# Performance work log

Measured on AMD Instinct MI355X. Metric: run time of the kernel, lower is better.

## Reference

```python
import jax, jax.numpy as jnp
import numpy as np


def _agcn(x, node_embeddings, weights_pool, bias_pool, supports):
    # per-node weights: [N, dim_in, dim_out]
    weights = jnp.einsum('nd,dio->nio', node_embeddings, weights_pool)
    bias = node_embeddings @ bias_pool  # [N, dim_out]
    x_g = jnp.einsum('nm,bmc->bnc', supports, x)  # adaptive-adjacency aggregation
    return jnp.einsum('bni,nio->bno', x_g, weights) + bias


def setup_inputs() -> dict:
    key = jax.random.key(0)
    ks = jax.random.split(key, 7)
    B, N, D_IN, D_OUT, E = 64, 4096, 64, 64, 16
    return {
        'x': jax.random.normal(ks[0], (B, N, D_IN), dtype=jnp.float32),
        'state': jax.random.normal(ks[1], (B, N, D_OUT), dtype=jnp.float32),
        'node_embeddings': jax.random.normal(ks[2], (N, E), dtype=jnp.float32),
        'gate_weights_pool': jax.random.normal(ks[3], (E, D_IN + D_OUT, 2 * D_OUT), dtype=jnp.float32) * 0.1,
        'gate_bias_pool': jax.random.normal(ks[4], (E, 2 * D_OUT), dtype=jnp.float32) * 0.1,
        'update_weights_pool': jax.random.normal(ks[5], (E, D_IN + D_OUT, D_OUT), dtype=jnp.float32) * 0.1,
        'update_bias_pool': jax.random.normal(ks[6], (E, D_OUT), dtype=jnp.float32) * 0.1,
    }


def reference(x, state, node_embeddings, gate_weights_pool, gate_bias_pool,
              update_weights_pool, update_bias_pool) -> jnp.ndarray:
    hidden_dim = state.shape[-1]
    # learned adjacency shared by both GCNs: softmax(relu(E E^T), axis=1)
    supports = jax.nn.softmax(jax.nn.relu(node_embeddings @ node_embeddings.T), axis=1)
    input_and_state = jnp.concatenate([x, state], axis=-1)  # [B,N,dim_in+hidden]
    z_r = jax.nn.sigmoid(_agcn(input_and_state, node_embeddings,
                               gate_weights_pool, gate_bias_pool, supports))
    z, r = z_r[..., :hidden_dim], z_r[..., hidden_dim:]
    candidate = jnp.concatenate([x, z * state], axis=-1)
    hc = jnp.tanh(_agcn(candidate, node_embeddings,
                        update_weights_pool, update_bias_pool, supports))
    h = r * state + (1.0 - r) * hc
    return h
```

## Files before the change

kernel.cpp:

```cpp
#include <hip/hip_runtime.h>

typedef float f32x4 __attribute__((ext_vector_type(4)));
typedef float f32x16 __attribute__((ext_vector_type(16)));
typedef _Float16 f16x8 __attribute__((ext_vector_type(8)));
typedef _Float16 f16x4 __attribute__((ext_vector_type(4)));
typedef _Float16 f16x2 __attribute__((ext_vector_type(2)));

typedef __attribute__((address_space(1))) const unsigned char gbyte;
typedef __attribute__((address_space(3))) unsigned char sbyte;
__device__ __forceinline__ void gload_lds16(const void* gp, void* lp) {
  __builtin_amdgcn_global_load_lds((gbyte*)gp, (sbyte*)lp, 16, 0, 0);
}

__global__ __launch_bounds__(256) void k_wpoolT(const float* __restrict__ gwp,
                                                const float* __restrict__ uwp,
                                                float* __restrict__ wtg,
                                                float* __restrict__ wtu) {
  int idx = blockIdx.x * 256 + threadIdx.x;
  if (idx < 16 * 128 * 128) {
    int d = idx >> 14, rem = idx & 16383, o = rem >> 7, i = rem & 127;
    wtg[idx] = gwp[(d << 14) + (i << 7) + o];
  } else {
    int j = idx - 16 * 128 * 128;
    if (j < 16 * 64 * 128) {
      int d = j >> 13, rem = j & 8191, o = rem >> 7, i = rem & 127;
      wtu[j] = uwp[(d << 13) + (i << 6) + o];
    }
  }
}

__global__ __launch_bounds__(256) void k_supports(const float* __restrict__ emb,
                                                  _Float16* __restrict__ S) {
  int n0 = blockIdx.x * 4, tid = threadIdx.x;
  __shared__ float e_sh[4][16];
  __shared__ float red[4][4];
  if (tid < 16) {
    int r = tid >> 2, part = tid & 3;
    f32x4 v = *reinterpret_cast<const f32x4*>(emb + (n0 + r) * 16 + part * 4);
    *reinterpret_cast<f32x4*>(&e_sh[r][part * 4]) = v;
  }
  __syncthreads();
  float v[4][16];
  float sum[4] = {0.f, 0.f, 0.f, 0.f};
#pragma unroll
  for (int i = 0; i < 16; i++) {
    int m = i * 256 + tid;
    const f32x4* em = reinterpret_cast<const f32x4*>(emb + m * 16);
    f32x4 e0 = em[0], e1 = em[1], e2 = em[2], e3 = em[3];
#pragma unroll
    for (int r = 0; r < 4; r++) {
      float acc = 0.f;
#pragma unroll
      for (int q = 0; q < 4; q++) acc += e_sh[r][q] * e0[q];
#pragma unroll
      for (int q = 0; q < 4; q++) acc += e_sh[r][4 + q] * e1[q];
#pragma unroll
      for (int q = 0; q < 4; q++) acc += e_sh[r][8 + q] * e2[q];
#pragma unroll
      for (int q = 0; q < 4; q++) acc += e_sh[r][12 + q] * e3[q];
      acc = fmaxf(acc, 0.f);
      float e = __expf(acc);
      v[r][i] = e;
      sum[r] += e;
    }
  }
#pragma unroll
  for (int r = 0; r < 4; r++)
#pragma unroll
    for (int off = 32; off > 0; off >>= 1) sum[r] += __shfl_down(sum[r], off);
  if ((tid & 63) == 0) {
#pragma unroll
    for (int r = 0; r < 4; r++) red[tid >> 6][r] = sum[r];
  }
  __syncthreads();
  float inv[4];
#pragma unroll
  for (int r = 0; r < 4; r++)
    inv[r] = 1.f / (red[0][r] + red[1][r] + red[2][r] + red[3][r]);
#pragma unroll
  for (int i = 0; i < 16; i++)
#pragma unroll
    for (int r = 0; r < 4; r++)
      S[(size_t)(n0 + r) * 4096 + i * 256 + tid] = (_Float16)(v[r][i] * inv[r]);
}

__global__ __launch_bounds__(256) void k_concat(const float* __restrict__ x,
                                                const float* __restrict__ st,
                                                _Float16* __restrict__ xs_t) {
  int m0 = blockIdx.x * 64, b = blockIdx.y, tid = threadIdx.x;
  __shared__ __attribute__((aligned(16))) _Float16 T[64][130];
#pragma unroll
  for (int i = 0; i < 16; i++) {
    int li = i * 256 + tid;
    int ml = li >> 6, c = li & 63;
    int base = (b * 4096 + m0 + ml) * 64 + c;
    T[ml][c] = (_Float16)x[base];
    T[ml][64 + c] = (_Float16)st[base];
  }
  __syncthreads();
  int cg = tid >> 3, mch = tid & 7;
#pragma unroll
  for (int cb = 0; cb < 4; cb++) {
    int c = cb * 32 + cg;
    f16x8 tmp;
#pragma unroll
    for (int j = 0; j < 8; j++) tmp[j] = T[mch * 8 + j][c];
    *reinterpret_cast<f16x8*>(&xs_t[(b * 128 + c) * 4096 + m0 + mch * 8]) = tmp;
  }
}

__global__ __launch_bounds__(512) void k_gemm(const _Float16* __restrict__ S,
                                              const _Float16* __restrict__ Xt,
                                              _Float16* __restrict__ Y) {
  int nt = blockIdx.x, b = blockIdx.y;
  int tid = threadIdx.x, lane = tid & 63, w = tid >> 6;
  int wr = w >> 1, wc = w & 1;
  __shared__ __attribute__((aligned(16))) _Float16 As[256 * 64];
  __shared__ __attribute__((aligned(16))) _Float16 Bs[128 * 64];
  const _Float16* Sb = S + (size_t)nt * 256 * 4096;
  const _Float16* Xb = Xt + (size_t)b * 128 * 4096;
  f32x16 acc[2][2];
#pragma unroll
  for (int fm = 0; fm < 2; fm++)
#pragma unroll
    for (int fn = 0; fn < 2; fn++)
#pragma unroll
      for (int q = 0; q < 16; q++) acc[fm][fn][q] = 0.f;

  int lrow = lane >> 3;
  int lcolsw = (((lane & 7) ^ lrow) * 8);
  int r32 = lane & 31, hi32 = lane >> 5;
  int swz = (r32 & 7) * 8;
  for (int k0 = 0; k0 < 4096; k0 += 64) {
    __syncthreads();
#pragma unroll
    for (int i = 0; i < 4; i++) {
      int j = w * 4 + i;
      int row = j * 8 + lrow;
      gload_lds16(Sb + (size_t)row * 4096 + k0 + lcolsw, &As[j * 512]);
    }
#pragma unroll
    for (int i = 0; i < 2; i++) {
      int j = w * 2 + i;
      int row = j * 8 + lrow;
      gload_lds16(Xb + (size_t)row * 4096 + k0 + lcolsw, &Bs[j * 512]);
    }
    __syncthreads();
#pragma unroll
    for (int kk = 0; kk < 4; kk++) {
      int col = (kk * 16 + hi32 * 8) ^ swz;
      f16x8 af[2], bf[2];
#pragma unroll
      for (int fm = 0; fm < 2; fm++)
        af[fm] = *reinterpret_cast<const f16x8*>(&As[(wr * 64 + fm * 32 + r32) * 64 + col]);
#pragma unroll
      for (int fn = 0; fn < 2; fn++)
        bf[fn] = *reinterpret_cast<const f16x8*>(&Bs[(wc * 64 + fn * 32 + r32) * 64 + col]);
#pragma unroll
      for (int fm = 0; fm < 2; fm++)
#pragma unroll
        for (int fn = 0; fn < 2; fn++)
          acc[fm][fn] = __builtin_amdgcn_mfma_f32_32x32x16_f16(af[fm], bf[fn], acc[fm][fn], 0, 0, 0);
    }
  }
#pragma unroll
  for (int fm = 0; fm < 2; fm++)
#pragma unroll
    for (int fn = 0; fn < 2; fn++)
#pragma unroll
      for (int reg = 0; reg < 16; reg++) {
        int row = nt * 256 + wr * 64 + fm * 32 + (reg & 3) + 8 * (reg >> 2) + 4 * hi32;
        int c = wc * 64 + fn * 32 + r32;
        Y[((size_t)row * 64 + b) * 128 + c] = (_Float16)acc[fm][fn][reg];
      }
}

__global__ __launch_bounds__(512) void k_gemm2(const _Float16* __restrict__ S,
                                               const _Float16* __restrict__ Xt,
                                               _Float16* __restrict__ Y) {
  int nt = blockIdx.x, bp = blockIdx.y;
  int tid = threadIdx.x, lane = tid & 63, w = tid >> 6;
  int wr = w >> 1, wc = w & 1;
  __shared__ __attribute__((aligned(16))) _Float16 As[256 * 64];
  __shared__ __attribute__((aligned(16))) _Float16 Bs[128 * 64];
  const _Float16* Sb = S + (size_t)nt * 256 * 4096;
  const _Float16* Xb = Xt + (size_t)(256 * bp + 64) * 4096;
  f32x16 acc[2][2];
#pragma unroll
  for (int fm = 0; fm < 2; fm++)
#pragma unroll
    for (int fn = 0; fn < 2; fn++)
#pragma unroll
      for (int q = 0; q < 16; q++) acc[fm][fn][q] = 0.f;

  int lrow = lane >> 3;
  int lcolsw = (((lane & 7) ^ lrow) * 8);
  int r32 = lane & 31, hi32 = lane >> 5;
  int swz = (r32 & 7) * 8;
  for (int k0 = 0; k0 < 4096; k0 += 64) {
    __syncthreads();
#pragma unroll
    for (int i = 0; i < 4; i++) {
      int j = w * 4 + i;
      int row = j * 8 + lrow;
      gload_lds16(Sb + (size_t)row * 4096 + k0 + lcolsw, &As[j * 512]);
    }
#pragma unroll
    for (int i = 0; i < 2; i++) {
      int j = w * 2 + i;
      int row = j * 8 + lrow;
      int groff = ((row >> 6) * 128 + (row & 63)) * 4096;
      gload_lds16(Xb + (size_t)groff + k0 + lcolsw, &Bs[j * 512]);
    }
    __syncthreads();
#pragma unroll
    for (int kk = 0; kk < 4; kk++) {
      int col = (kk * 16 + hi32 * 8) ^ swz;
      f16x8 af[2], bf[2];
#pragma unroll
      for (int fm = 0; fm < 2; fm++)
        af[fm] = *reinterpret_cast<const f16x8*>(&As[(wr * 64 + fm * 32 + r32) * 64 + col]);
#pragma unroll
      for (int fn = 0; fn < 2; fn++)
        bf[fn] = *reinterpret_cast<const f16x8*>(&Bs[(wc * 64 + fn * 32 + r32) * 64 + col]);
#pragma unroll
      for (int fm = 0; fm < 2; fm++)
#pragma unroll
        for (int fn = 0; fn < 2; fn++)
          acc[fm][fn] = __builtin_amdgcn_mfma_f32_32x32x16_f16(af[fm], bf[fn], acc[fm][fn], 0, 0, 0);
    }
  }
#pragma unroll
  for (int fm = 0; fm < 2; fm++)
#pragma unroll
    for (int fn = 0; fn < 2; fn++)
#pragma unroll
      for (int reg = 0; reg < 16; reg++) {
        int row = nt * 256 + wr * 64 + fm * 32 + (reg & 3) + 8 * (reg >> 2) + 4 * hi32;
        int ct = wc * 64 + fn * 32 + r32;
        int batch = 2 * bp + (ct >> 6);
        int c = 64 + (ct & 63);
        Y[((size_t)row * 64 + batch) * 128 + c] = (_Float16)acc[fm][fn][reg];
      }
}

__global__ __launch_bounds__(256) void k_wall(const float* __restrict__ emb, int n0,
                                              const float* __restrict__ wt, int OI,
                                              _Float16* __restrict__ Wout) {
  int bx = blockIdx.x, by = blockIdx.y, tid = threadIdx.x;
  __shared__ float e_sh[64][16];
  {
    int node = tid >> 2, part = tid & 3;
    f32x4 v = *reinterpret_cast<const f32x4*>(emb + (n0 + bx * 64 + node) * 16 + part * 4);
    *reinterpret_cast<f32x4*>(&e_sh[node][part * 4]) = v;
  }
  __syncthreads();
  int oi0 = by * 2048 + tid * 8;
#pragma unroll
  for (int g = 0; g < 8; g++) {
    f32x4 a0[8], a1[8];
#pragma unroll
    for (int nn = 0; nn < 8; nn++) { a0[nn] = (f32x4){0,0,0,0}; a1[nn] = (f32x4){0,0,0,0}; }
#pragma unroll
    for (int d = 0; d < 16; d++) {
      const f32x4* p = reinterpret_cast<const f32x4*>(wt + d * OI + oi0);
      f32x4 v0 = p[0], v1 = p[1];
#pragma unroll
      for (int nn = 0; nn < 8; nn++) {
        float e = e_sh[g * 8 + nn][d];
        a0[nn] += e * v0;
        a1[nn] += e * v1;
      }
    }
#pragma unroll
    for (int nn = 0; nn < 8; nn++) {
      f16x8 pk;
#pragma unroll
      for (int q = 0; q < 4; q++) { pk[q] = (_Float16)a0[nn][q]; pk[4 + q] = (_Float16)a1[nn][q]; }
      int node = bx * 64 + g * 8 + nn;
      *reinterpret_cast<f16x8*>(Wout + (size_t)node * OI + oi0) = pk;
    }
  }
}

__global__ __launch_bounds__(256) void k_gate(const _Float16* __restrict__ xg,
                                              const float* __restrict__ emb,
                                              const _Float16* __restrict__ Wc,
                                              const float* __restrict__ gbp,
                                              int n0,
                                              _Float16* __restrict__ zb,
                                              _Float16* __restrict__ rb) {
  int n = n0 + blockIdx.x, tid = threadIdx.x, lane = tid & 63, w = tid >> 6;
  __shared__ __attribute__((aligned(16))) _Float16 As[64 * 64];
  __shared__ __attribute__((aligned(16))) _Float16 Bs[128 * 64];
  __shared__ float bias_sh[128];
  const _Float16* wrow = Wc + (size_t)blockIdx.x * 16384;
  const _Float16* arow = xg + (size_t)n * 8192;
  if (tid < 128) {
    float s = 0.f;
#pragma unroll
    for (int d = 0; d < 16; d++) s += emb[n * 16 + d] * gbp[d * 128 + tid];
    bias_sh[tid] = s;
  }
  f32x16 acc[2];
#pragma unroll
  for (int fm = 0; fm < 2; fm++)
#pragma unroll
    for (int q = 0; q < 16; q++) acc[fm][q] = 0.f;

  int lrow = lane >> 3;
  int lcolsw = (((lane & 7) ^ lrow) * 8);
  int r32 = lane & 31, hi32 = lane >> 5;
  int swz = (r32 & 7) * 8;
  for (int k0 = 0; k0 < 128; k0 += 64) {
    __syncthreads();
#pragma unroll
    for (int i = 0; i < 2; i++) {
      int j = w * 2 + i;
      int row = j * 8 + lrow;
      gload_lds16(arow + row * 128 + k0 + lcolsw, &As[j * 512]);
    }
#pragma unroll
    for (int i = 0; i < 4; i++) {
      int j = w * 4 + i;
      int row = j * 8 + lrow;
      gload_lds16(wrow + row * 128 + k0 + lcolsw, &Bs[j * 512]);
    }
    __syncthreads();
#pragma unroll
    for (int kk = 0; kk < 4; kk++) {
      int col = (kk * 16 + hi32 * 8) ^ swz;
      f16x8 bf = *reinterpret_cast<const f16x8*>(&Bs[(w * 32 + r32) * 64 + col]);
#pragma unroll
      for (int fm = 0; fm < 2; fm++) {
        f16x8 af = *reinterpret_cast<const f16x8*>(&As[(fm * 32 + r32) * 64 + col]);
        acc[fm] = __builtin_amdgcn_mfma_f32_32x32x16_f16(af, bf, acc[fm], 0, 0, 0);
      }
    }
  }
  int o = w * 32 + r32;
  float bias = bias_sh[o];
#pragma unroll
  for (int fm = 0; fm < 2; fm++)
#pragma unroll
    for (int reg = 0; reg < 16; reg++) {
      int brow = fm * 32 + (reg & 3) + 8 * (reg >> 2) + 4 * hi32;
      float val = acc[fm][reg] + bias;
      float sg = 1.f / (1.f + __expf(-val));
      if (o < 64) zb[(n * 64 + brow) * 64 + o] = (_Float16)sg;
      else        rb[(n * 64 + brow) * 64 + (o - 64)] = (_Float16)sg;
    }
}

__global__ __launch_bounds__(256) void k_cand(const _Float16* __restrict__ zb,
                                              const float* __restrict__ st,
                                              _Float16* __restrict__ xs_t) {
  int m0 = blockIdx.x * 64, b = blockIdx.y, tid = threadIdx.x;
  __shared__ __attribute__((aligned(16))) _Float16 T[64][66];
#pragma unroll
  for (int i = 0; i < 16; i++) {
    int li = i * 256 + tid, ml = li >> 6, o = li & 63;
    float z = (float)zb[((m0 + ml) * 64 + b) * 64 + o];
    float s = st[(b * 4096 + m0 + ml) * 64 + o];
    T[ml][o] = (_Float16)(z * s);
  }
  __syncthreads();
  int og = tid >> 3, mch = tid & 7;
#pragma unroll
  for (int cb = 0; cb < 2; cb++) {
    int o = cb * 32 + og;
    f16x8 tmp;
#pragma unroll
    for (int j = 0; j < 8; j++) tmp[j] = T[mch * 8 + j][o];
    *reinterpret_cast<f16x8*>(&xs_t[(b * 128 + 64 + o) * 4096 + m0 + mch * 8]) = tmp;
  }
}

__global__ __launch_bounds__(256) void k_upd(const _Float16* __restrict__ xg2,
                                             const float* __restrict__ emb,
                                             const _Float16* __restrict__ Wc,
                                             const float* __restrict__ ubp,
                                             const _Float16* __restrict__ rb,
                                             const float* __restrict__ st,
                                             float* __restrict__ out) {
  int n = blockIdx.x, tid = threadIdx.x, lane = tid & 63, w = tid >> 6;
  int fm = w >> 1, fn = w & 1;
  __shared__ __attribute__((aligned(16))) _Float16 As[64 * 64];
  __shared__ __attribute__((aligned(16))) _Float16 Bs[64 * 64];
  __shared__ float bias_sh[64];
  const _Float16* wrow = Wc + (size_t)n * 8192;
  const _Float16* arow = xg2 + (size_t)n * 8192;
  if (tid < 64) {
    float s = 0.f;
#pragma unroll
    for (int d = 0; d < 16; d++) s += emb[n * 16 + d] * ubp[d * 64 + tid];
    bias_sh[tid] = s;
  }
  f32x16 acc;
#pragma unroll
  for (int q = 0; q < 16; q++) acc[q] = 0.f;

  int lrow = lane >> 3;
  int lcolsw = (((lane & 7) ^ lrow) * 8);
  int r32 = lane & 31, hi32 = lane >> 5;
  int swz = (r32 & 7) * 8;
  for (int k0 = 0; k0 < 128; k0 += 64) {
    __syncthreads();
#pragma unroll
    for (int i = 0; i < 2; i++) {
      int j = w * 2 + i;
      int row = j * 8 + lrow;
      gload_lds16(arow + row * 128 + k0 + lcolsw, &As[j * 512]);
    }
#pragma unroll
    for (int i = 0; i < 2; i++) {
      int j = w * 2 + i;
      int row = j * 8 + lrow;
      gload_lds16(wrow + row * 128 + k0 + lcolsw, &Bs[j * 512]);
    }
    __syncthreads();
#pragma unroll
    for (int kk = 0; kk < 4; kk++) {
      int col = (kk * 16 + hi32 * 8) ^ swz;
      f16x8 af = *reinterpret_cast<const f16x8*>(&As[(fm * 32 + r32) * 64 + col]);
      f16x8 bf = *reinterpret_cast<const f16x8*>(&Bs[(fn * 32 + r32) * 64 + col]);
      acc = __builtin_amdgcn_mfma_f32_32x32x16_f16(af, bf, acc, 0, 0, 0);
    }
  }
  int o = fn * 32 + r32;
  float bias = bias_sh[o];
#pragma unroll
  for (int reg = 0; reg < 16; reg++) {
    int brow = fm * 32 + (reg & 3) + 8 * (reg >> 2) + 4 * hi32;
    float val = acc[reg] + bias;
    float e2 = __expf(2.f * val);
    float hc = 1.f - 2.f / (e2 + 1.f);
    float rr = (float)rb[(n * 64 + brow) * 64 + o];
    float s = st[((size_t)brow * 4096 + n) * 64 + o];
    out[((size_t)brow * 4096 + n) * 64 + o] = rr * s + (1.f - rr) * hc;
  }
}

extern "C" void kernel_launch(void* const* d_in, const int* in_sizes, int n_in,
                              void* d_out, int out_size, void* d_ws, size_t ws_size,
                              hipStream_t stream) {
  const float* x   = (const float*)d_in[0];
  const float* st  = (const float*)d_in[1];
  const float* emb = (const float*)d_in[2];
  const float* gwp = (const float*)d_in[3];
  const float* gbp = (const float*)d_in[4];
  const float* uwp = (const float*)d_in[5];
  const float* ubp = (const float*)d_in[6];
  float* out = (float*)d_out;
  char* ws = (char*)d_ws;

  _Float16* slotA = (_Float16*)(ws + 0);
  _Float16* xs_t  = (_Float16*)(ws + 33554432);
  _Float16* xg    = (_Float16*)(ws + 100663296);
  _Float16* zb    = (_Float16*)(ws + 167772160);
  _Float16* rb    = (_Float16*)(ws + 201326592);
  float* wtg = (float*)(ws + 234881024);
  float* wtu = (float*)(ws + 235929600);
  if (ws_size < 236453888ull) return;

  k_wpoolT<<<1536, 256, 0, stream>>>(gwp, uwp, wtg, wtu);
  k_supports<<<1024, 256, 0, stream>>>(emb, slotA);
  k_concat<<<dim3(64, 64), 256, 0, stream>>>(x, st, xs_t);
  k_gemm<<<dim3(16, 64), 512, 0, stream>>>(slotA, xs_t, xg);
  for (int c = 0; c < 2; c++) {
    k_wall<<<dim3(32, 8), 256, 0, stream>>>(emb, c * 2048, wtg, 16384, xs_t);
    k_gate<<<2048, 256, 0, stream>>>(xg, emb, xs_t, gbp, c * 2048, zb, rb);
  }
  k_cand<<<dim3(64, 64), 256, 0, stream>>>(zb, st, xs_t);
  k_gemm2<<<dim3(16, 32), 512, 0, stream>>>(slotA, xs_t, xg);
  k_wall<<<dim3(64, 4), 256, 0, stream>>>(emb, 0, wtu, 8192, xs_t);
  k_upd<<<4096, 256, 0, stream>>>(xg, emb, xs_t, ubp, rb, st, out);
}
```

Baseline: 703.4 us.

## Triple-buffer LDS tiles in k_gemm to overlap global loads with MFMA

Converts the single-buffered LDS staging in the support×X GEMM into a three-stage ring. Two tiles are prefetched ahead with direct global-to-LDS loads, and each iteration waits on a partial vmcnt before a single barrier. The goal is to hide global memory latency behind the MFMA work and to drop one of the two barriers per k-step. In exchange, LDS use per block triples to 144 KB, which limits occupancy to one block per CU and depends on correct hand-written waitcnt accounting.

```diff
diff --git a/kernel.cpp b/kernel.cpp
--- a/kernel.cpp
+++ b/kernel.cpp
@@ -115,8 +115,8 @@
   int nt = blockIdx.x, b = blockIdx.y;
   int tid = threadIdx.x, lane = tid & 63, w = tid >> 6;
   int wr = w >> 1, wc = w & 1;
-  __shared__ __attribute__((aligned(16))) _Float16 As[256 * 64];
-  __shared__ __attribute__((aligned(16))) _Float16 Bs[128 * 64];
+  __shared__ __attribute__((aligned(16))) _Float16 As[3][256 * 64];
+  __shared__ __attribute__((aligned(16))) _Float16 Bs[3][128 * 64];
   const _Float16* Sb = S + (size_t)nt * 256 * 4096;
   const _Float16* Xb = Xt + (size_t)b * 128 * 4096;
   f32x16 acc[2][2];
@@ -131,31 +131,46 @@
   int lcolsw = (((lane & 7) ^ lrow) * 8);
   int r32 = lane & 31, hi32 = lane >> 5;
   int swz = (r32 & 7) * 8;
-  for (int k0 = 0; k0 < 4096; k0 += 64) {
-    __syncthreads();
+
+  auto STAGE = [&](int v, int k0) {
 #pragma unroll
     for (int i = 0; i < 4; i++) {
       int j = w * 4 + i;
       int row = j * 8 + lrow;
-      gload_lds16(Sb + (size_t)row * 4096 + k0 + lcolsw, &As[j * 512]);
+      gload_lds16(Sb + (size_t)row * 4096 + k0 + lcolsw, &As[v][j * 512]);
     }
 #pragma unroll
     for (int i = 0; i < 2; i++) {
       int j = w * 2 + i;
       int row = j * 8 + lrow;
-      gload_lds16(Xb + (size_t)row * 4096 + k0 + lcolsw, &Bs[j * 512]);
-    }
-    __syncthreads();
+      gload_lds16(Xb + (size_t)row * 4096 + k0 + lcolsw, &Bs[v][j * 512]);
+    }
+  };
+
+  STAGE(0, 0);
+  STAGE(1, 64);
+  for (int t = 0; t < 64; ++t) {
+    if (t < 63) {
+      asm volatile("s_waitcnt vmcnt(6)" ::: "memory");
+    } else {
+      asm volatile("s_waitcnt vmcnt(0)" ::: "memory");
+    }
+    __builtin_amdgcn_sched_barrier(0);
+    __builtin_amdgcn_s_barrier();
+    __builtin_amdgcn_sched_barrier(0);
+    if (t + 2 < 64) STAGE((t + 2) % 3, (t + 2) * 64);
+    const _Float16* Av = As[t % 3];
+    const _Float16* Bv = Bs[t % 3];
 #pragma unroll
     for (int kk = 0; kk < 4; kk++) {
       int col = (kk * 16 + hi32 * 8) ^ swz;
       f16x8 af[2], bf[2];
 #pragma unroll
       for (int fm = 0; fm < 2; fm++)
-        af[fm] = *reinterpret_cast<const f16x8*>(&As[(wr * 64 + fm * 32 + r32) * 64 + col]);
+        af[fm] = *reinterpret_cast<const f16x8*>(&Av[(wr * 64 + fm * 32 + r32) * 64 + col]);
 #pragma unroll
       for (int fn = 0; fn < 2; fn++)
-        bf[fn] = *reinterpret_cast<const f16x8*>(&Bs[(wc * 64 + fn * 32 + r32) * 64 + col]);
+        bf[fn] = *reinterpret_cast<const f16x8*>(&Bv[(wc * 64 + fn * 32 + r32) * 64 + col]);
 #pragma unroll
       for (int fm = 0; fm < 2; fm++)
 #pragma unroll
```

Result: slower. 780.6 us (+11.0%).
